# Performance work log

Measured on AMD Instinct MI355X. Metric: run time of the kernel, lower is better.

Reference implementation:

```python
import jax, jax.numpy as jnp
import numpy as np


def setup_inputs() -> dict:
    key = jax.random.key(0)
    k1, k2 = jax.random.split(key)
    B, C, R, I, O = 64, 16, 1152, 64, 64
    x = jax.random.normal(k1, (B, R, I), dtype=jnp.float32)
    route_weights = jax.random.normal(k2, (C, R, I, O), dtype=jnp.float32)
    route_logits = jnp.zeros((C, 1, R, 1, 1), dtype=jnp.float32)
    return {"x": x, "route_weights": route_weights, "route_logits": route_logits}


def _squash(t, axis=-1):
    # scale = |t|^2 / (1 + |t|^2); out = scale * t / |t|  (no epsilon, faithful to source)
    sq = jnp.sum(t * t, axis=axis, keepdims=True)
    return (sq / (1.0 + sq)) * t / jnp.sqrt(sq)


def reference(x, route_weights, route_logits):
    NUM_ITERS = 3
    # priors: (C, B, R, 1, O)
    priors = jnp.einsum('bri,crio->cbro', x, route_weights)[:, :, :, None, :]
    logits = route_logits  # (C, 1, R, 1, 1), broadcasts over batch
    outputs = None
    for i in range(NUM_ITERS):
        probs = jax.nn.softmax(logits, axis=2)          # softmax over route nodes
        s = jnp.sum(probs * priors, axis=2, keepdims=True)  # (C, B, 1, 1, O)
        outputs = _squash(s, axis=-1)
        if i != NUM_ITERS - 1:
            # delta logits: agreement between priors and outputs
            logits = logits + jnp.sum(priors * outputs, axis=-1, keepdims=True)
    return outputs  # (C, B, 1, 1, O)
```

## Files before the change

kernel.cpp:

```cpp
#include <hip/hip_runtime.h>
#include <math.h>

#define Cc 16
#define Bb 64
#define Rr 1152
#define Ii 64
#define Oo 64
#define RT 8

static __device__ __forceinline__ float4 ld4(const float* p){ return *reinterpret_cast<const float4*>(p); }
static __device__ __forceinline__ void st4(float* p, float4 v){ *reinterpret_cast<float4*>(p) = v; }

__device__ float gProbs0[Cc*Rr];
__device__ float gS[Cc*Bb*Oo];
__device__ float gOut[Cc*Bb*Oo];
__device__ float gL1[(size_t)Cc*Bb*Rr];
__device__ float gLp[(size_t)Cc*Bb*Rr];

__global__ void kz_zeroS(){
  const int i = blockIdx.x*256 + threadIdx.x;
  if (i < Cc*Bb*Oo) gS[i] = 0.f;
}

static __device__ void softmax_row(const float* __restrict__ L, float* __restrict__ out,
                                   float* __restrict__ sred ){
  const int tid = threadIdx.x;
  float m = -3.4e38f;
  for (int r = tid; r < Rr; r += 256) m = fmaxf(m, L[r]);
  #pragma unroll
  for (int off = 1; off < 64; off <<= 1) m = fmaxf(m, __shfl_xor(m, off));
  if ((tid & 63) == 0) sred[tid >> 6] = m;
  __syncthreads();
  m = fmaxf(fmaxf(sred[0], sred[1]), fmaxf(sred[2], sred[3]));
  float s = 0.f;
  for (int r = tid; r < Rr; r += 256) s += __expf(L[r] - m);
  #pragma unroll
  for (int off = 1; off < 64; off <<= 1) s += __shfl_xor(s, off);
  if ((tid & 63) == 0) sred[4 + (tid >> 6)] = s;
  __syncthreads();
  s = sred[4] + sred[5] + sred[6] + sred[7];
  const float inv = 1.0f / s;
  for (int r = tid; r < Rr; r += 256) out[r] = __expf(L[r] - m) * inv;
}

__global__ void k0f(const float* __restrict__ lg){
  __shared__ float sred[8];
  const int c = blockIdx.x;
  softmax_row(lg + c*Rr, gProbs0 + c*Rr, sred);
}

static __device__ __forceinline__ void fma_row(float4& a, const float4 xv,
    const float4 w0, const float4 w1, const float4 w2, const float4 w3){
  a.x = fmaf(xv.x, w0.x, fmaf(xv.y, w1.x, fmaf(xv.z, w2.x, fmaf(xv.w, w3.x, a.x))));
  a.y = fmaf(xv.x, w0.y, fmaf(xv.y, w1.y, fmaf(xv.z, w2.y, fmaf(xv.w, w3.y, a.y))));
  a.z = fmaf(xv.x, w0.z, fmaf(xv.y, w1.z, fmaf(xv.z, w2.z, fmaf(xv.w, w3.z, a.z))));
  a.w = fmaf(xv.x, w0.w, fmaf(xv.y, w1.w, fmaf(xv.z, w2.w, fmaf(xv.w, w3.w, a.w))));
}

static __device__ void stage_gemm(const float* __restrict__ x, const float* __restrict__ w,
                                  int c, int r, int tid, int tb, int to,
                                  float* __restrict__ Xs, float* __restrict__ Ws,
                                  float4* __restrict__ acc){
  const float4* wsrc = reinterpret_cast<const float4*>(w + (size_t)(c*Rr + r) * (Ii*Oo));
  #pragma unroll
  for (int qq = 0; qq < 4; ++qq) {
    const int fi = tid + 256*qq;
    reinterpret_cast<float4*>(Ws)[fi] = wsrc[fi];
    const int b  = fi >> 4;
    const int i4 = (fi & 15) << 2;
    st4(&Xs[b*68 + i4], ld4(x + (size_t)(b*Rr + r)*Ii + i4));
  }
  __syncthreads();
  #pragma unroll
  for (int j = 0; j < 4; ++j) acc[j] = make_float4(0.f,0.f,0.f,0.f);
  #pragma unroll
  for (int i4 = 0; i4 < Ii; i4 += 4) {
    const float4 xv0 = ld4(&Xs[(tb+0)*68 + i4]);
    const float4 xv1 = ld4(&Xs[(tb+1)*68 + i4]);
    const float4 xv2 = ld4(&Xs[(tb+2)*68 + i4]);
    const float4 xv3 = ld4(&Xs[(tb+3)*68 + i4]);
    const float4 wv0 = ld4(&Ws[(i4+0)*64 + to]);
    const float4 wv1 = ld4(&Ws[(i4+1)*64 + to]);
    const float4 wv2 = ld4(&Ws[(i4+2)*64 + to]);
    const float4 wv3 = ld4(&Ws[(i4+3)*64 + to]);
    fma_row(acc[0], xv0, wv0, wv1, wv2, wv3);
    fma_row(acc[1], xv1, wv0, wv1, wv2, wv3);
    fma_row(acc[2], xv2, wv0, wv1, wv2, wv3);
    fma_row(acc[3], xv3, wv0, wv1, wv2, wv3);
  }
}

__launch_bounds__(256)
__global__ void k1_priors(const float* __restrict__ x, const float* __restrict__ w,
                          float* __restrict__ P){
  const int c   = blockIdx.x;
  const int r0  = blockIdx.y * RT;
  const int tid = threadIdx.x;
  const int to  = (tid & 15) * 4;
  const int tb  = (tid >> 4) * 4;
  __shared__ float Xs[64*68];
  __shared__ float Ws[64*64];

  float4 s0a[4];
  #pragma unroll
  for (int j = 0; j < 4; ++j) s0a[j] = make_float4(0.f,0.f,0.f,0.f);

  for (int rr = 0; rr < RT; ++rr) {
    const int r = r0 + rr;
    float4 acc[4];
    stage_gemm(x, w, c, r, tid, tb, to, Xs, Ws, acc);
    const float pr = gProbs0[c*Rr + r];
    #pragma unroll
    for (int j = 0; j < 4; ++j) {
      st4(&P[((size_t)(c*Bb + tb + j)*Rr + r)*Oo + to], acc[j]);
      s0a[j].x = fmaf(pr, acc[j].x, s0a[j].x);
      s0a[j].y = fmaf(pr, acc[j].y, s0a[j].y);
      s0a[j].z = fmaf(pr, acc[j].z, s0a[j].z);
      s0a[j].w = fmaf(pr, acc[j].w, s0a[j].w);
    }
    __syncthreads();
  }
  #pragma unroll
  for (int j = 0; j < 4; ++j) {
    float* dst = &gS[(size_t)(c*Bb + tb + j)*Oo + to];
    atomicAdd(dst + 0, s0a[j].x);
    atomicAdd(dst + 1, s0a[j].y);
    atomicAdd(dst + 2, s0a[j].z);
    atomicAdd(dst + 3, s0a[j].w);
  }
}

__launch_bounds__(256)
__global__ void k3_routing(const float* __restrict__ P, const float* __restrict__ lg0g,
                           float* __restrict__ out){
  const int b = blockIdx.x, c = blockIdx.y;
  const int tid  = threadIdx.x;
  const int wv   = tid >> 6;
  const int lane = tid & 63;
  const int g    = lane >> 4;
  const int q    = lane & 15;
  const int o4   = q * 4;
  const int pid  = wv*4 + g;

  __shared__ float lg0[Rr];
  __shared__ float lgs1[Rr];
  __shared__ float outv[Oo];
  __shared__ float marr[16], larr[16];
  __shared__ float sarr[16*Oo];

  for (int r = tid; r < Rr; r += 256) lg0[r] = lg0g[c*Rr + r];

  if (tid < 64) {
    const float s = gS[(size_t)(c*Bb + b)*Oo + tid];
    float t2 = s*s;
    #pragma unroll
    for (int off = 1; off < 64; off <<= 1) t2 += __shfl_xor(t2, off);
    outv[tid] = s * (t2 / ((1.0f + t2) * sqrtf(t2)));
  }
  __syncthreads();

  const float4* Pcb = reinterpret_cast<const float4*>(P + (size_t)(c*Bb + b)*Rr*Oo);

  #pragma unroll 1
  for (int pass = 1; pass <= 2; ++pass) {
    float m = -3.4e38f, l = 0.f;
    float4 sa = make_float4(0.f,0.f,0.f,0.f);
    const float4 ov = ld4(&outv[o4]);

    for (int step = 0; step < Rr/16; ++step) {
      const int r = step*16 + wv*4 + g;
      const float4 pv = Pcb[r*16 + q];
      float d = pv.x*ov.x + pv.y*ov.y + pv.z*ov.z + pv.w*ov.w;
      d += __shfl_xor(d, 1);
      d += __shfl_xor(d, 2);
      d += __shfl_xor(d, 4);
      d += __shfl_xor(d, 8);
      const float base = (pass == 1) ? lg0[r] : lgs1[r];
      const float lgt  = base + d;
      if (pass == 1 && q == 0) lgs1[r] = lgt;
      const float nm = fmaxf(m, lgt);
      const float wo = __expf(m - nm);
      const float wn = __expf(lgt - nm);
      l = l*wo + wn;
      sa.x = fmaf(pv.x, wn, sa.x*wo);
      sa.y = fmaf(pv.y, wn, sa.y*wo);
      sa.z = fmaf(pv.z, wn, sa.z*wo);
      sa.w = fmaf(pv.w, wn, sa.w*wo);
      m = nm;
    }

    if (q == 0) { marr[pid] = m; larr[pid] = l; }
    st4(&sarr[pid*Oo + o4], sa);
    __syncthreads();

    if (tid < 64) {
      float M = -3.4e38f;
      #pragma unroll
      for (int p = 0; p < 16; ++p) M = fmaxf(M, marr[p]);
      float L = 0.f, sv = 0.f;
      #pragma unroll
      for (int p = 0; p < 16; ++p) {
        const float f = __expf(marr[p] - M);
        L += larr[p] * f;
        sv += sarr[p*Oo + tid] * f;
      }
      const float s = sv / L;
      float t2 = s*s;
      #pragma unroll
      for (int off = 1; off < 64; off <<= 1) t2 += __shfl_xor(t2, off);
      outv[tid] = s * (t2 / ((1.0f + t2) * sqrtf(t2)));
    }
    __syncthreads();
  }

  if (tid < 64) out[(size_t)(c*Bb + b)*Oo + tid] = outv[tid];
}

__launch_bounds__(256)
__global__ void kf_sum(const float* __restrict__ x, const float* __restrict__ w, int which){
  const int c   = blockIdx.x;
  const int r0  = blockIdx.y * RT;
  const int tid = threadIdx.x;
  const int to  = (tid & 15) * 4;
  const int tb  = (tid >> 4) * 4;
  __shared__ float Xs[64*68];
  __shared__ float Ws[64*64];
  const float* pcbr = (which == 1) ? gLp : gL1;

  float4 sa[4];
  #pragma unroll
  for (int j = 0; j < 4; ++j) sa[j] = make_float4(0.f,0.f,0.f,0.f);

  for (int rr = 0; rr < RT; ++rr) {
    const int r = r0 + rr;
    float4 acc[4];
    stage_gemm(x, w, c, r, tid, tb, to, Xs, Ws, acc);
    #pragma unroll
    for (int j = 0; j < 4; ++j) {
      const float wt = (which == 0) ? gProbs0[c*Rr + r]
                                    : pcbr[(size_t)(c*Bb + tb + j)*Rr + r];
      sa[j].x = fmaf(wt, acc[j].x, sa[j].x);
      sa[j].y = fmaf(wt, acc[j].y, sa[j].y);
      sa[j].z = fmaf(wt, acc[j].z, sa[j].z);
      sa[j].w = fmaf(wt, acc[j].w, sa[j].w);
    }
    __syncthreads();
  }
  #pragma unroll
  for (int j = 0; j < 4; ++j) {
    float* dst = &gS[(size_t)(c*Bb + tb + j)*Oo + to];
    atomicAdd(dst + 0, sa[j].x);
    atomicAdd(dst + 1, sa[j].y);
    atomicAdd(dst + 2, sa[j].z);
    atomicAdd(dst + 3, sa[j].w);
  }
}

__launch_bounds__(256)
__global__ void kf_delta(const float* __restrict__ x, const float* __restrict__ w,
                         const float* __restrict__ lg, int pass){
  const int c   = blockIdx.x;
  const int r0  = blockIdx.y * RT;
  const int tid = threadIdx.x;
  const int to  = (tid & 15) * 4;
  const int tb  = (tid >> 4) * 4;
  __shared__ float Xs[64*68];
  __shared__ float Ws[64*64];
  float* dst = (pass == 1) ? gL1 : gLp;

  float4 ov[4];
  #pragma unroll
  for (int j = 0; j < 4; ++j) ov[j] = ld4(&gOut[(size_t)(c*Bb + tb + j)*Oo + to]);

  for (int rr = 0; rr < RT; ++rr) {
    const int r = r0 + rr;
    float4 acc[4];
    stage_gemm(x, w, c, r, tid, tb, to, Xs, Ws, acc);
    float pd[4];
    #pragma unroll
    for (int j = 0; j < 4; ++j) {
      float d = acc[j].x*ov[j].x + acc[j].y*ov[j].y + acc[j].z*ov[j].z + acc[j].w*ov[j].w;
      d += __shfl_xor(d, 1);
      d += __shfl_xor(d, 2);
      d += __shfl_xor(d, 4);
      d += __shfl_xor(d, 8);
      pd[j] = d;
    }
    if ((tid & 15) == 0) {
      #pragma unroll
      for (int j = 0; j < 4; ++j) {
        const size_t li = (size_t)(c*Bb + tb + j)*Rr + r;
        const float base = (pass == 1) ? lg[c*Rr + r] : gL1[li];
        dst[li] = base + pd[j];
      }
    }
    __syncthreads();
  }
}

__global__ void kf_softmax(int dir){
  __shared__ float sred[8];
  const size_t idx = blockIdx.x;
  const float* src = (dir == 0) ? gL1 : gLp;
  float*       dst = (dir == 0) ? gLp : gL1;
  softmax_row(src + idx*Rr, dst + idx*Rr, sred);
}

__global__ void kf_squash(float* __restrict__ out, int toFinal){
  const size_t idx = blockIdx.x;
  const int t = threadIdx.x;
  const float s = gS[idx*Oo + t];
  float t2 = s*s;
  #pragma unroll
  for (int off = 1; off < 64; off <<= 1) t2 += __shfl_xor(t2, off);
  float* dst = toFinal ? out : gOut;
  dst[idx*Oo + t] = s * (t2 / ((1.0f + t2) * sqrtf(t2)));
}

extern "C" void kernel_launch(void* const* d_in, const int* in_sizes, int n_in,
                              void* d_out, int out_size, void* d_ws, size_t ws_size,
                              hipStream_t stream) {
  const float* x  = (const float*)d_in[0];
  const float* w  = (const float*)d_in[1];
  const float* lg = (const float*)d_in[2];
  float* out = (float*)d_out;

  const dim3 gTiles(Cc, Rr/RT);
  const int  zb = (Cc*Bb*Oo + 255)/256;

  kz_zeroS<<<dim3(zb), 256, 0, stream>>>();
  k0f<<<dim3(Cc), 256, 0, stream>>>(lg);

  const size_t needP = (size_t)Cc*Bb*Rr*Oo*sizeof(float);
  if (ws_size >= needP) {
    float* P = (float*)d_ws;
    k1_priors<<<gTiles, 256, 0, stream>>>(x, w, P);
    k3_routing<<<dim3(Bb, Cc), 256, 0, stream>>>(P, lg, out);
  } else {
    kf_sum   <<<gTiles, 256, 0, stream>>>(x, w, 0);
    kf_squash<<<dim3(Cc*Bb), 64, 0, stream>>>(out, 0);
    kf_delta <<<gTiles, 256, 0, stream>>>(x, w, lg, 1);
    kf_softmax<<<dim3(Cc*Bb), 256, 0, stream>>>(0);
    kz_zeroS <<<dim3(zb), 256, 0, stream>>>();
    kf_sum   <<<gTiles, 256, 0, stream>>>(x, w, 1);
    kf_squash<<<dim3(Cc*Bb), 64, 0, stream>>>(out, 0);
    kf_delta <<<gTiles, 256, 0, stream>>>(x, w, lg, 2);
    kf_softmax<<<dim3(Cc*Bb), 256, 0, stream>>>(1);
    kz_zeroS <<<dim3(zb), 256, 0, stream>>>();
    kf_sum   <<<gTiles, 256, 0, stream>>>(x, w, 2);
    kf_squash<<<dim3(Cc*Bb), 64, 0, stream>>>(out, 1);
  }
}
```

Baseline: 693.2 us.

## Chunk capsules to shrink priors buffer, async LDS loads, deterministic partial-sum reduce

The priors path now processes capsules in chunks of four, so the materialized priors buffer is a quarter of the size and has a better chance of staying in the large last-level cache between the GEMM and routing kernels. The priors GEMM double-buffers weight and input tiles with direct global-to-LDS loads and an XOR swizzle, and writes per-block partial sums instead of using float atomics. A new reduce kernel squashes those partials, and the routing kernel uses 512 threads with four rows in flight per iteration. The cost is more kernel launches and an extra partial-sum round trip, and the workspace need changes, which decides which path runs.

New measurement: 632.3 us. 1.1x faster.

```diff
diff --git a/kernel.cpp b/kernel.cpp
--- a/kernel.cpp
+++ b/kernel.cpp
@@ -6,10 +6,19 @@
 #define Rr 1152
 #define Ii 64
 #define Oo 64
-#define RT 8
+#define CH 4
+#define NRB 128
+#define RT 9
+#define RTF 8
 
 static __device__ __forceinline__ float4 ld4(const float* p){ return *reinterpret_cast<const float4*>(p); }
 static __device__ __forceinline__ void st4(float* p, float4 v){ *reinterpret_cast<float4*>(p) = v; }
+
+static __device__ __forceinline__ void gl_lds16(const float4* g, float4* l){
+  __builtin_amdgcn_global_load_lds(
+      (const __attribute__((address_space(1))) void*)g,
+      (__attribute__((address_space(3))) void*)l, 16, 0, 0);
+}
 
 __device__ float gProbs0[Cc*Rr];
 __device__ float gS[Cc*Bb*Oo];
@@ -23,7 +32,7 @@
 }
 
 static __device__ void softmax_row(const float* __restrict__ L, float* __restrict__ out,
-                                   float* __restrict__ sred ){
+                                   float* __restrict__ sred){
   const int tid = threadIdx.x;
   float m = -3.4e38f;
   for (int r = tid; r < Rr; r += 256) m = fmaxf(m, L[r]);
@@ -45,8 +54,11 @@
 
 __global__ void k0f(const float* __restrict__ lg){
   __shared__ float sred[8];
-  const int c = blockIdx.x;
-  softmax_row(lg + c*Rr, gProbs0 + c*Rr, sred);
+  softmax_row(lg + blockIdx.x*Rr, gProbs0 + blockIdx.x*Rr, sred);
+}
+__global__ void k0p(const float* __restrict__ lg, float* __restrict__ pr){
+  __shared__ float sred[8];
+  softmax_row(lg + blockIdx.x*Rr, pr + blockIdx.x*Rr, sred);
 }
 
 static __device__ __forceinline__ void fma_row(float4& a, const float4 xv,
@@ -55,6 +67,221 @@
   a.y = fmaf(xv.x, w0.y, fmaf(xv.y, w1.y, fmaf(xv.z, w2.y, fmaf(xv.w, w3.y, a.y))));
   a.z = fmaf(xv.x, w0.z, fmaf(xv.y, w1.z, fmaf(xv.z, w2.z, fmaf(xv.w, w3.z, a.z))));
   a.w = fmaf(xv.x, w0.w, fmaf(xv.y, w1.w, fmaf(xv.z, w2.w, fmaf(xv.w, w3.w, a.w))));
+}
+
+static __device__ __forceinline__ void stage_async(const float4* __restrict__ xsrc,
+    const float4* __restrict__ wsrc, int r, int wv, int ln,
+    float4* __restrict__ Wb, float4* __restrict__ Xb){
+  #pragma unroll
+  for (int qq = 0; qq < 4; ++qq) {
+    const int base = (wv*4 + qq) * 64;
+    const int p    = base + ln;
+    gl_lds16(wsrc + p, Wb + base);
+    const int b  = p >> 4;
+    const int lc = (p & 15) ^ ((b >> 2) & 3);
+    gl_lds16(xsrc + (((size_t)(b*Rr + r)) << 4) + lc, Xb + base);
+  }
+}
+
+__launch_bounds__(256)
+__global__ void k1_priors(const float* __restrict__ x, const float* __restrict__ w,
+                          const float* __restrict__ probs0, int c0,
+                          float* __restrict__ P, float* __restrict__ Sp){
+  const int ci  = blockIdx.x;
+  const int c   = c0 + ci;
+  const int rb  = blockIdx.y;
+  const int r0  = rb * RT;
+  const int tid = threadIdx.x;
+  const int q   = tid & 15;
+  const int to  = q * 4;
+  const int tb  = (tid >> 4) * 4;
+  const int wv  = tid >> 6;
+  const int ln  = tid & 63;
+  const int sx  = (tb >> 2) & 3;
+
+  __shared__ float4 Wl[2][1024];
+  __shared__ float4 Xl[2][1024];
+
+  const float4* xsrc = reinterpret_cast<const float4*>(x);
+
+  float4 s0a[4];
+  #pragma unroll
+  for (int j = 0; j < 4; ++j) s0a[j] = make_float4(0.f,0.f,0.f,0.f);
+
+  int buf = 0;
+  stage_async(xsrc, reinterpret_cast<const float4*>(w) + (size_t)(c*Rr + r0)*1024,
+              r0, wv, ln, Wl[0], Xl[0]);
+  __syncthreads();
+
+  for (int rr = 0; rr < RT; ++rr) {
+    const int r = r0 + rr;
+    if (rr + 1 < RT)
+      stage_async(xsrc, reinterpret_cast<const float4*>(w) + (size_t)(c*Rr + r + 1)*1024,
+                  r + 1, wv, ln, Wl[buf^1], Xl[buf^1]);
+
+    const float4* W4 = Wl[buf];
+    const float4* X4 = Xl[buf];
+    float4 acc0 = make_float4(0.f,0.f,0.f,0.f);
+    float4 acc1 = acc0, acc2 = acc0, acc3 = acc0;
+
+    #pragma unroll
+    for (int kg = 0; kg < 16; ++kg) {
+      const float4 wv0 = W4[(kg*4+0)*16 + q];
+      const float4 wv1 = W4[(kg*4+1)*16 + q];
+      const float4 wv2 = W4[(kg*4+2)*16 + q];
+      const float4 wv3 = W4[(kg*4+3)*16 + q];
+      const int xc = kg ^ sx;
+      const float4 xv0 = X4[(tb+0)*16 + xc];
+      const float4 xv1 = X4[(tb+1)*16 + xc];
+      const float4 xv2 = X4[(tb+2)*16 + xc];
+      const float4 xv3 = X4[(tb+3)*16 + xc];
+      fma_row(acc0, xv0, wv0, wv1, wv2, wv3);
+      fma_row(acc1, xv1, wv0, wv1, wv2, wv3);
+      fma_row(acc2, xv2, wv0, wv1, wv2, wv3);
+      fma_row(acc3, xv3, wv0, wv1, wv2, wv3);
+    }
+
+    const float pr = probs0[c*Rr + r];
+    st4(&P[(((size_t)(ci*Bb + tb+0))*Rr + r)*Oo + to], acc0);
+    st4(&P[(((size_t)(ci*Bb + tb+1))*Rr + r)*Oo + to], acc1);
+    st4(&P[(((size_t)(ci*Bb + tb+2))*Rr + r)*Oo + to], acc2);
+    st4(&P[(((size_t)(ci*Bb + tb+3))*Rr + r)*Oo + to], acc3);
+    s0a[0].x = fmaf(pr, acc0.x, s0a[0].x); s0a[0].y = fmaf(pr, acc0.y, s0a[0].y);
+    s0a[0].z = fmaf(pr, acc0.z, s0a[0].z); s0a[0].w = fmaf(pr, acc0.w, s0a[0].w);
+    s0a[1].x = fmaf(pr, acc1.x, s0a[1].x); s0a[1].y = fmaf(pr, acc1.y, s0a[1].y);
+    s0a[1].z = fmaf(pr, acc1.z, s0a[1].z); s0a[1].w = fmaf(pr, acc1.w, s0a[1].w);
+    s0a[2].x = fmaf(pr, acc2.x, s0a[2].x); s0a[2].y = fmaf(pr, acc2.y, s0a[2].y);
+    s0a[2].z = fmaf(pr, acc2.z, s0a[2].z); s0a[2].w = fmaf(pr, acc2.w, s0a[2].w);
+    s0a[3].x = fmaf(pr, acc3.x, s0a[3].x); s0a[3].y = fmaf(pr, acc3.y, s0a[3].y);
+    s0a[3].z = fmaf(pr, acc3.z, s0a[3].z); s0a[3].w = fmaf(pr, acc3.w, s0a[3].w);
+
+    __syncthreads();
+    buf ^= 1;
+  }
+
+  #pragma unroll
+  for (int j = 0; j < 4; ++j)
+    st4(&Sp[((((size_t)ci*NRB) + rb)*Bb + tb + j)*Oo + to], s0a[j]);
+}
+
+__launch_bounds__(256)
+__global__ void k2_reduce(const float* __restrict__ Sp, float* __restrict__ out0){
+  const int blk = blockIdx.x;
+  const int ci  = blk >> 6, b = blk & 63;
+  const int wv  = threadIdx.x >> 6, o = threadIdx.x & 63;
+  __shared__ float part[4][64];
+  float s = 0.f;
+  #pragma unroll 4
+  for (int rb = wv*32; rb < wv*32 + 32; ++rb)
+    s += Sp[((((size_t)ci*NRB) + rb)*Bb + b)*Oo + o];
+  part[wv][o] = s;
+  __syncthreads();
+  if (threadIdx.x < 64) {
+    s = part[0][o] + part[1][o] + part[2][o] + part[3][o];
+    float t2 = s*s;
+    #pragma unroll
+    for (int off = 1; off < 64; off <<= 1) t2 += __shfl_xor(t2, off);
+    out0[(size_t)blk*Oo + o] = s * (t2 / ((1.0f + t2) * sqrtf(t2)));
+  }
+}
+
+__launch_bounds__(512)
+__global__ void k3_routing(const float* __restrict__ P, const float* __restrict__ out0,
+                           const float* __restrict__ lg0g, int c0,
+                           float* __restrict__ out){
+  const int b   = blockIdx.x;
+  const int ci  = blockIdx.y;
+  const int c   = c0 + ci;
+  const int tid = threadIdx.x;
+  const int wv  = tid >> 6;
+  const int ln  = tid & 63;
+  const int g   = ln >> 4;
+  const int q   = ln & 15;
+  const int o4  = q * 4;
+  const int pid = wv*4 + g;
+
+  __shared__ float lg0[Rr];
+  __shared__ float lgs1[Rr];
+  __shared__ float outv[Oo];
+  __shared__ float marr[32], larr[32];
+  __shared__ float sarr[32*Oo];
+
+  for (int r = tid; r < Rr; r += 512) lg0[r] = lg0g[c*Rr + r];
+  if (tid < 64) outv[tid] = out0[((size_t)(ci*Bb + b))*Oo + tid];
+  __syncthreads();
+
+  const float4* Pcb = reinterpret_cast<const float4*>(P) + ((size_t)(ci*Bb + b))*Rr*16;
+  const int rbase = wv*4 + g;
+
+  #pragma unroll 1
+  for (int pass = 1; pass <= 2; ++pass) {
+    float m = -3.4e38f, l = 0.f;
+    float4 sa = make_float4(0.f,0.f,0.f,0.f);
+    const float4 ov = ld4(&outv[o4]);
+
+    #pragma unroll 1
+    for (int it = 0; it < 9; ++it) {
+      const int r0i = it*128 + rbase;
+      const float4 pv0 = Pcb[(r0i +  0)*16 + q];
+      const float4 pv1 = Pcb[(r0i + 32)*16 + q];
+      const float4 pv2 = Pcb[(r0i + 64)*16 + q];
+      const float4 pv3 = Pcb[(r0i + 96)*16 + q];
+
+      float d0 = pv0.x*ov.x + pv0.y*ov.y + pv0.z*ov.z + pv0.w*ov.w;
+      float d1 = pv1.x*ov.x + pv1.y*ov.y + pv1.z*ov.z + pv1.w*ov.w;
+      float d2 = pv2.x*ov.x + pv2.y*ov.y + pv2.z*ov.z + pv2.w*ov.w;
+      float d3 = pv3.x*ov.x + pv3.y*ov.y + pv3.z*ov.z + pv3.w*ov.w;
+      #pragma unroll
+      for (int off = 1; off < 16; off <<= 1) {
+        d0 += __shfl_xor(d0, off);
+        d1 += __shfl_xor(d1, off);
+        d2 += __shfl_xor(d2, off);
+        d3 += __shfl_xor(d3, off);
+      }
+      float b0, b1, b2, b3;
+      if (pass == 1) { b0 = lg0[r0i]; b1 = lg0[r0i+32]; b2 = lg0[r0i+64]; b3 = lg0[r0i+96]; }
+      else           { b0 = lgs1[r0i]; b1 = lgs1[r0i+32]; b2 = lgs1[r0i+64]; b3 = lgs1[r0i+96]; }
+      const float l0 = b0 + d0, l1 = b1 + d1, l2 = b2 + d2, l3 = b3 + d3;
+      if (pass == 1 && q == 0) {
+        lgs1[r0i] = l0; lgs1[r0i+32] = l1; lgs1[r0i+64] = l2; lgs1[r0i+96] = l3;
+      }
+      const float mx = fmaxf(fmaxf(fmaxf(l0, l1), fmaxf(l2, l3)), m);
+      const float wo = __expf(m - mx);
+      const float e0 = __expf(l0 - mx), e1 = __expf(l1 - mx);
+      const float e2 = __expf(l2 - mx), e3 = __expf(l3 - mx);
+      l = l*wo + e0 + e1 + e2 + e3;
+      sa.x = fmaf(pv0.x, e0, fmaf(pv1.x, e1, fmaf(pv2.x, e2, fmaf(pv3.x, e3, sa.x*wo))));
+      sa.y = fmaf(pv0.y, e0, fmaf(pv1.y, e1, fmaf(pv2.y, e2, fmaf(pv3.y, e3, sa.y*wo))));
+      sa.z = fmaf(pv0.z, e0, fmaf(pv1.z, e1, fmaf(pv2.z, e2, fmaf(pv3.z, e3, sa.z*wo))));
+      sa.w = fmaf(pv0.w, e0, fmaf(pv1.w, e1, fmaf(pv2.w, e2, fmaf(pv3.w, e3, sa.w*wo))));
+      m = mx;
+    }
+
+    if (q == 0) { marr[pid] = m; larr[pid] = l; }
+    st4(&sarr[pid*Oo + o4], sa);
+    __syncthreads();
+
+    if (tid < 64) {
+      float M = -3.4e38f;
+      #pragma unroll
+      for (int p = 0; p < 32; ++p) M = fmaxf(M, marr[p]);
+      float L = 0.f, sv = 0.f;
+      #pragma unroll
+      for (int p = 0; p < 32; ++p) {
+        const float f = __expf(marr[p] - M);
+        L += larr[p] * f;
+        sv = fmaf(sarr[p*Oo + tid], f, sv);
+      }
+      const float s = sv / L;
+      float t2 = s*s;
+      #pragma unroll
+      for (int off = 1; off < 64; off <<= 1) t2 += __shfl_xor(t2, off);
+      outv[tid] = s * (t2 / ((1.0f + t2) * sqrtf(t2)));
+    }
+    __syncthreads();
+  }
+
+  if (tid < 64) out[((size_t)c*Bb + b)*Oo + tid] = outv[tid];
 }
 
 static __device__ void stage_gemm(const float* __restrict__ x, const float* __restrict__ w,
@@ -91,147 +318,16 @@
 }
 
 __launch_bounds__(256)
-__global__ void k1_priors(const float* __restrict__ x, const float* __restrict__ w,
-                          float* __restrict__ P){
-  const int c   = blockIdx.x;
-  const int r0  = blockIdx.y * RT;
-  const int tid = threadIdx.x;
-  const int to  = (tid & 15) * 4;
-  const int tb  = (tid >> 4) * 4;
-  __shared__ float Xs[64*68];
-  __shared__ float Ws[64*64];
-
-  float4 s0a[4];
-  #pragma unroll
-  for (int j = 0; j < 4; ++j) s0a[j] = make_float4(0.f,0.f,0.f,0.f);
-
-  for (int rr = 0; rr < RT; ++rr) {
-    const int r = r0 + rr;
-    float4 acc[4];
-    stage_gemm(x, w, c, r, tid, tb, to, Xs, Ws, acc);
-    const float pr = gProbs0[c*Rr + r];
-    #pragma unroll
-    for (int j = 0; j < 4; ++j) {
-      st4(&P[((size_t)(c*Bb + tb + j)*Rr + r)*Oo + to], acc[j]);
-      s0a[j].x = fmaf(pr, acc[j].x, s0a[j].x);
-      s0a[j].y = fmaf(pr, acc[j].y, s0a[j].y);
-      s0a[j].z = fmaf(pr, acc[j].z, s0a[j].z);
-      s0a[j].w = fmaf(pr, acc[j].w, s0a[j].w);
-    }
-    __syncthreads();
-  }
-  #pragma unroll
-  for (int j = 0; j < 4; ++j) {
-    float* dst = &gS[(size_t)(c*Bb + tb + j)*Oo + to];
-    atomicAdd(dst + 0, s0a[j].x);
-    atomicAdd(dst + 1, s0a[j].y);
-    atomicAdd(dst + 2, s0a[j].z);
-    atomicAdd(dst + 3, s0a[j].w);
-  }
-}
-
-__launch_bounds__(256)
-__global__ void k3_routing(const float* __restrict__ P, const float* __restrict__ lg0g,
-                           float* __restrict__ out){
-  const int b = blockIdx.x, c = blockIdx.y;
-  const int tid  = threadIdx.x;
-  const int wv   = tid >> 6;
-  const int lane = tid & 63;
-  const int g    = lane >> 4;
-  const int q    = lane & 15;
-  const int o4   = q * 4;
-  const int pid  = wv*4 + g;
-
-  __shared__ float lg0[Rr];
-  __shared__ float lgs1[Rr];
-  __shared__ float outv[Oo];
-  __shared__ float marr[16], larr[16];
-  __shared__ float sarr[16*Oo];
-
-  for (int r = tid; r < Rr; r += 256) lg0[r] = lg0g[c*Rr + r];
-
-  if (tid < 64) {
-    const float s = gS[(size_t)(c*Bb + b)*Oo + tid];
-    float t2 = s*s;
-    #pragma unroll
-    for (int off = 1; off < 64; off <<= 1) t2 += __shfl_xor(t2, off);
-    outv[tid] = s * (t2 / ((1.0f + t2) * sqrtf(t2)));
-  }
-  __syncthreads();
-
-  const float4* Pcb = reinterpret_cast<const float4*>(P + (size_t)(c*Bb + b)*Rr*Oo);
-
-  #pragma unroll 1
-  for (int pass = 1; pass <= 2; ++pass) {
-    float m = -3.4e38f, l = 0.f;
-    float4 sa = make_float4(0.f,0.f,0.f,0.f);
-    const float4 ov = ld4(&outv[o4]);
-
-    for (int step = 0; step < Rr/16; ++step) {
-      const int r = step*16 + wv*4 + g;
-      const float4 pv = Pcb[r*16 + q];
-      float d = pv.x*ov.x + pv.y*ov.y + pv.z*ov.z + pv.w*ov.w;
-      d += __shfl_xor(d, 1);
-      d += __shfl_xor(d, 2);
-      d += __shfl_xor(d, 4);
-      d += __shfl_xor(d, 8);
-      const float base = (pass == 1) ? lg0[r] : lgs1[r];
-      const float lgt  = base + d;
-      if (pass == 1 && q == 0) lgs1[r] = lgt;
-      const float nm = fmaxf(m, lgt);
-      const float wo = __expf(m - nm);
-      const float wn = __expf(lgt - nm);
-      l = l*wo + wn;
-      sa.x = fmaf(pv.x, wn, sa.x*wo);
-      sa.y = fmaf(pv.y, wn, sa.y*wo);
-      sa.z = fmaf(pv.z, wn, sa.z*wo);
-      sa.w = fmaf(pv.w, wn, sa.w*wo);
-      m = nm;
-    }
-
-    if (q == 0) { marr[pid] = m; larr[pid] = l; }
-    st4(&sarr[pid*Oo + o4], sa);
-    __syncthreads();
-
-    if (tid < 64) {
-      float M = -3.4e38f;
-      #pragma unroll
-      for (int p = 0; p < 16; ++p) M = fmaxf(M, marr[p]);
-      float L = 0.f, sv = 0.f;
-      #pragma unroll
-      for (int p = 0; p < 16; ++p) {
-        const float f = __expf(marr[p] - M);
-        L += larr[p] * f;
-        sv += sarr[p*Oo + tid] * f;
-      }
-      const float s = sv / L;
-      float t2 = s*s;
-      #pragma unroll
-      for (int off = 1; off < 64; off <<= 1) t2 += __shfl_xor(t2, off);
-      outv[tid] = s * (t2 / ((1.0f + t2) * sqrtf(t2)));
-    }
-    __syncthreads();
-  }
-
-  if (tid < 64) out[(size_t)(c*Bb + b)*Oo + tid] = outv[tid];
-}
-
-__launch_bounds__(256)
 __global__ void kf_sum(const float* __restrict__ x, const float* __restrict__ w, int which){
-  const int c   = blockIdx.x;
-  const int r0  = blockIdx.y * RT;
-  const int tid = threadIdx.x;
-  const int to  = (tid & 15) * 4;
-  const int tb  = (tid >> 4) * 4;
+  const int c = blockIdx.x, r0 = blockIdx.y * RTF, tid = threadIdx.x;
+  const int to = (tid & 15) * 4, tb = (tid >> 4) * 4;
   __shared__ float Xs[64*68];
   __shared__ float Ws[64*64];
   const float* pcbr = (which == 1) ? gLp : gL1;
-
   float4 sa[4];
   #pragma unroll
   for (int j = 0; j < 4; ++j) sa[j] = make_float4(0.f,0.f,0.f,0.f);
-
-  for (int rr = 0; rr < RT; ++rr) {
+  for (int rr = 0; rr < RTF; ++rr) {
     const int r = r0 + rr;
     float4 acc[4];
     stage_gemm(x, w, c, r, tid, tb, to, Xs, Ws, acc);
@@ -259,20 +355,15 @@
 __launch_bounds__(256)
 __global__ void kf_delta(const float* __restrict__ x, const float* __restrict__ w,
                          const float* __restrict__ lg, int pass){
-  const int c   = blockIdx.x;
-  const int r0  = blockIdx.y * RT;
-  const int tid = threadIdx.x;
-  const int to  = (tid & 15) * 4;
-  const int tb  = (tid >> 4) * 4;
+  const int c = blockIdx.x, r0 = blockIdx.y * RTF, tid = threadIdx.x;
+  const int to = (tid & 15) * 4, tb = (tid >> 4) * 4;
   __shared__ float Xs[64*68];
   __shared__ float Ws[64*64];
   float* dst = (pass == 1) ? gL1 : gLp;
-
   float4 ov[4];
   #pragma unroll
   for (int j = 0; j < 4; ++j) ov[j] = ld4(&gOut[(size_t)(c*Bb + tb + j)*Oo + to]);
-
-  for (int rr = 0; rr < RT; ++rr) {
+  for (int rr = 0; rr < RTF; ++rr) {
     const int r = r0 + rr;
     float4 acc[4];
     stage_gemm(x, w, c, r, tid, tb, to, Xs, Ws, acc);
@@ -280,10 +371,8 @@
     #pragma unroll
     for (int j = 0; j < 4; ++j) {
       float d = acc[j].x*ov[j].x + acc[j].y*ov[j].y + acc[j].z*ov[j].z + acc[j].w*ov[j].w;
-      d += __shfl_xor(d, 1);
-      d += __shfl_xor(d, 2);
-      d += __shfl_xor(d, 4);
-      d += __shfl_xor(d, 8);
+      d += __shfl_xor(d, 1); d += __shfl_xor(d, 2);
+      d += __shfl_xor(d, 4); d += __shfl_xor(d, 8);
       pd[j] = d;
     }
     if ((tid & 15) == 0) {
@@ -324,19 +413,30 @@
   const float* w  = (const float*)d_in[1];
   const float* lg = (const float*)d_in[2];
   float* out = (float*)d_out;
-
-  const dim3 gTiles(Cc, Rr/RT);
-  const int  zb = (Cc*Bb*Oo + 255)/256;
-
-  kz_zeroS<<<dim3(zb), 256, 0, stream>>>();
-  k0f<<<dim3(Cc), 256, 0, stream>>>(lg);
-
-  const size_t needP = (size_t)Cc*Bb*Rr*Oo*sizeof(float);
-  if (ws_size >= needP) {
-    float* P = (float*)d_ws;
-    k1_priors<<<gTiles, 256, 0, stream>>>(x, w, P);
-    k3_routing<<<dim3(Bb, Cc), 256, 0, stream>>>(P, lg, out);
+  float* ws  = (float*)d_ws;
+
+  const size_t nP  = (size_t)CH*Bb*Rr*Oo;
+  const size_t nSp = (size_t)CH*NRB*Bb*Oo;
+  const size_t nO0 = (size_t)CH*Bb*Oo;
+  const size_t nPr = (size_t)Cc*Rr;
+  const size_t need = (nP + nSp + nO0 + nPr) * sizeof(float);
+
+  if (ws_size >= need) {
+    float* P   = ws;
+    float* Sp  = P + nP;
+    float* o0  = Sp + nSp;
+    float* pr  = o0 + nO0;
+    k0p<<<dim3(Cc), 256, 0, stream>>>(lg, pr);
+    for (int c0 = 0; c0 < Cc; c0 += CH) {
+      k1_priors<<<dim3(CH, NRB), 256, 0, stream>>>(x, w, pr, c0, P, Sp);
+      k2_reduce<<<dim3(CH*Bb), 256, 0, stream>>>(Sp, o0);
+      k3_routing<<<dim3(Bb, CH), 512, 0, stream>>>(P, o0, lg, c0, out);
+    }
   } else {
+    const dim3 gTiles(Cc, Rr/RTF);
+    const int  zb = (Cc*Bb*Oo + 255)/256;
+    kz_zeroS<<<dim3(zb), 256, 0, stream>>>();
+    k0f<<<dim3(Cc), 256, 0, stream>>>(lg);
     kf_sum   <<<gTiles, 256, 0, stream>>>(x, w, 0);
     kf_squash<<<dim3(Cc*Bb), 64, 0, stream>>>(out, 0);
     kf_delta <<<gTiles, 256, 0, stream>>>(x, w, lg, 1);
```
